# Performance work log

Measured on AMD Instinct MI355X. Metric: run time of the kernel, lower is better.

## Reference

```python
import jax, jax.numpy as jnp
import numpy as np

N_TOKENS = 65536   # number of embeddings to quantize
CODE_DIM = 768     # embedding dim
NUM_CODES = 4096   # codebook size


def setup_inputs() -> dict:
    key = jax.random.key(0)
    k1, k2 = jax.random.split(key)
    x = jax.random.normal(k1, (N_TOKENS, CODE_DIM), dtype=jnp.float32)
    codebook = jax.random.normal(k2, (NUM_CODES, CODE_DIM), dtype=jnp.float32)
    return {"x": x, "codebook": codebook}


def reference(x, codebook):
    # argmin over squared distances == argmin over cdist (sqrt is monotone).
    x2 = jnp.sum(x * x, axis=-1, keepdims=True)          # [N, 1]
    c2 = jnp.sum(codebook * codebook, axis=-1)           # [K]
    dist = x2 + c2[None, :] - 2.0 * jnp.einsum('nd,kd->nk', x, codebook)  # [N, K]
    indices = jnp.argmin(dist, axis=-1)                  # [N] int
    quantized = codebook[indices]                        # gather [N, D]
    # straight-through estimator: forward = quantized, grad flows to x
    q_ste = x + jax.lax.stop_gradient(quantized - x)
    return q_ste, indices
```

## Files before the change

kernel.cpp:

```cpp
#include <hip/hip_runtime.h>

#define N_TOKENS  65536
#define CODE_DIM  768
#define NUM_CODES 4096

#define MARGIN 0.12f
#define FLTMAX 3.4028235e38f

typedef __attribute__((ext_vector_type(8))) _Float16 f16x8;
typedef __attribute__((ext_vector_type(4))) float f32x4;

__device__ __forceinline__ unsigned short f2h(float f) {
  _Float16 h = (_Float16)f;
  return *(unsigned short*)&h;
}
__device__ __forceinline__ void gl2lds16(const void* g, void* l) {
  __builtin_amdgcn_global_load_lds(
      (const __attribute__((address_space(1))) unsigned int*)g,
      (__attribute__((address_space(3))) unsigned int*)l, 16, 0, 0);
}

__global__ __launch_bounds__(256) void vq_convert_kernel(
    const float* __restrict__ x, const float* __restrict__ cb,
    unsigned short* __restrict__ xh, unsigned short* __restrict__ ch,
    float* __restrict__ x2, float* __restrict__ c2, int* __restrict__ fcnt) {
  if (blockIdx.x == 0 && threadIdx.x == 0) *fcnt = 0;
  const int wave = threadIdx.x >> 6;
  const int lane = threadIdx.x & 63;
  const int row  = blockIdx.x * 4 + wave;
  const float* src;
  unsigned short* hdst;
  float* ndst;
  if (row < N_TOKENS) {
    src = x + (size_t)row * CODE_DIM;
    hdst = xh + (size_t)row * CODE_DIM;
    ndst = x2 + row;
  } else {
    const int r = row - N_TOKENS;
    if (r >= NUM_CODES) return;
    src = cb + (size_t)r * CODE_DIM;
    hdst = ch + (size_t)r * CODE_DIM;
    ndst = c2 + r;
  }
  const float4* s4 = (const float4*)src;
  ushort4* h4 = (ushort4*)hdst;
  float acc = 0.f;
#pragma unroll
  for (int i = 0; i < 3; ++i) {
    float4 f = s4[lane + 64 * i];
    ushort4 h;
    h.x = f2h(f.x); h.y = f2h(f.y); h.z = f2h(f.z); h.w = f2h(f.w);
    h4[lane + 64 * i] = h;
    acc += (f.x * f.x + f.y * f.y) + (f.z * f.z + f.w * f.w);
  }
#pragma unroll
  for (int off = 32; off > 0; off >>= 1) acc += __shfl_down(acc, off, 64);
  if (lane == 0) *ndst = acc;
}

#define BT 256
#define KTILE 256
#define NKT (NUM_CODES / KTILE)
#define NST (CODE_DIM / 64)
#define TOT (NKT * NST)

__global__ __launch_bounds__(512, 2) void vq_mfma_kernel(
    const unsigned short* __restrict__ xh, const unsigned short* __restrict__ ch,
    const float* __restrict__ c2, int* __restrict__ out_idx,
    int* __restrict__ fcnt, int* __restrict__ flist) {
  __shared__ __align__(16) unsigned short sA[2][BT * 64];
  __shared__ __align__(16) unsigned short sB[2][KTILE * 64];
  __shared__ float redv[512], redsv[512];
  __shared__ int   redi[512];

  const int tid = threadIdx.x;
  const int wave = tid >> 6, lane = tid & 63;
  const int l15 = lane & 15, quad = lane >> 4;
  const int wr = wave >> 1, wc = wave & 1;
  const int tokBase = blockIdx.x * BT;

  const int lr = lane >> 3;
  const int cSrc = (lane & 7) ^ lr;
  const size_t aOff = (size_t)(tokBase + wave * 32 + lr) * CODE_DIM + cSrc * 8;
  const size_t bOff = (size_t)(wave * 32 + lr) * CODE_DIM + cSrc * 8;

  const int apos = (quad ^ (l15 & 7)) * 8;
  const int aB0 = (wr * 64 + l15) * 64 + apos;
  const int aB1 = (wr * 64 + l15) * 64 + (apos ^ 32);
  const int bB0 = (wc * 128 + l15) * 64 + apos;
  const int bB1 = (wc * 128 + l15) * 64 + (apos ^ 32);

  float v[4][4], sv[4][4];
  int bi[4][4];
#pragma unroll
  for (int i = 0; i < 4; ++i)
#pragma unroll
    for (int r = 0; r < 4; ++r) { v[i][r] = FLTMAX; sv[i][r] = FLTMAX; bi[i][r] = 0; }

  auto STAGE = [&](int slot, int s) {
    const int kw = (s % NST) * 64;
    const size_t rb = (size_t)(s / NST) * (KTILE * (size_t)CODE_DIM);
#pragma unroll
    for (int t = 0; t < 4; ++t)
      gl2lds16(xh + aOff + (size_t)t * (8 * CODE_DIM) + kw,
               &sA[slot][(wave * 32 + t * 8) * 64]);
#pragma unroll
    for (int t = 0; t < 4; ++t)
      gl2lds16(ch + rb + bOff + (size_t)t * (8 * CODE_DIM) + kw,
               &sB[slot][(wave * 32 + t * 8) * 64]);
  };

  STAGE(0, 0);
  asm volatile("s_waitcnt vmcnt(0)" ::: "memory");
  __builtin_amdgcn_s_barrier();
  __builtin_amdgcn_sched_barrier(0);

  for (int kt = 0; kt < NKT; ++kt) {
    f32x4 acc[4][8];
#pragma unroll
    for (int i = 0; i < 4; ++i)
#pragma unroll
      for (int j = 0; j < 8; ++j) acc[i][j] = (f32x4){0.f, 0.f, 0.f, 0.f};

    for (int ks = 0; ks < NST; ++ks) {
      const int gstep = kt * NST + ks;
      const int cur = gstep & 1;
      const unsigned short* As = sA[cur];
      const unsigned short* Bs = sB[cur];
      if (gstep < TOT - 1) STAGE(cur ^ 1, gstep + 1);

      f16x8 fa[4], fb[8];
#pragma unroll
      for (int i = 0; i < 4; ++i) fa[i] = *(const f16x8*)(As + aB0 + i * 1024);
#pragma unroll
      for (int j = 0; j < 8; ++j) fb[j] = *(const f16x8*)(Bs + bB0 + j * 1024);
      __builtin_amdgcn_s_setprio(1);
#pragma unroll
      for (int i = 0; i < 4; ++i)
#pragma unroll
        for (int j = 0; j < 8; ++j)
          acc[i][j] = __builtin_amdgcn_mfma_f32_16x16x32_f16(fa[i], fb[j], acc[i][j], 0, 0, 0);
      __builtin_amdgcn_s_setprio(0);
#pragma unroll
      for (int i = 0; i < 4; ++i) fa[i] = *(const f16x8*)(As + aB1 + i * 1024);
#pragma unroll
      for (int j = 0; j < 8; ++j) fb[j] = *(const f16x8*)(Bs + bB1 + j * 1024);
      __builtin_amdgcn_s_setprio(1);
#pragma unroll
      for (int i = 0; i < 4; ++i)
#pragma unroll
        for (int j = 0; j < 8; ++j)
          acc[i][j] = __builtin_amdgcn_mfma_f32_16x16x32_f16(fa[i], fb[j], acc[i][j], 0, 0, 0);
      __builtin_amdgcn_s_setprio(0);

      asm volatile("s_waitcnt vmcnt(0)" ::: "memory");
      __builtin_amdgcn_s_barrier();
      __builtin_amdgcn_sched_barrier(0);
    }

    const int kbase = kt * KTILE;
#pragma unroll
    for (int j = 0; j < 8; ++j) {
      const int kcol = kbase + wc * 128 + j * 16 + l15;
      const float c2j = c2[kcol];
#pragma unroll
      for (int i = 0; i < 4; ++i)
#pragma unroll
        for (int r = 0; r < 4; ++r) {
          float s = fmaf(-2.0f, acc[i][j][r], c2j);
          float vo = v[i][r];
          sv[i][r] = fminf(sv[i][r], fmaxf(s, vo));
          bool lt = s < vo;
          v[i][r]  = lt ? s : vo;
          bi[i][r] = lt ? kcol : bi[i][r];
        }
    }
  }

#pragma unroll
  for (int i = 0; i < 4; ++i)
#pragma unroll
    for (int r = 0; r < 4; ++r) {
      float vv = v[i][r], svv = sv[i][r];
      int ii = bi[i][r];
#pragma unroll
      for (int m = 1; m < 16; m <<= 1) {
        float ov = __shfl_xor(vv, m, 64);
        float osv = __shfl_xor(svv, m, 64);
        int oi = __shfl_xor(ii, m, 64);
        float nsv = fminf(fminf(svv, osv), fmaxf(vv, ov));
        bool take = (ov < vv) || (ov == vv && oi < ii);
        vv = take ? ov : vv;
        ii = take ? oi : ii;
        svv = nsv;
      }
      if (l15 == 0) {
        int row = wr * 64 + i * 16 + quad * 4 + r;
        redv[row * 2 + wc] = vv;
        redsv[row * 2 + wc] = svv;
        redi[row * 2 + wc] = ii;
      }
    }
  __syncthreads();
  if (tid < 256) {
    float v0 = redv[tid * 2], v1 = redv[tid * 2 + 1];
    float s0 = redsv[tid * 2], s1 = redsv[tid * 2 + 1];
    int i0 = redi[tid * 2], i1 = redi[tid * 2 + 1];
    bool take = (v1 < v0) || (v1 == v0 && i1 < i0);
    float bv = take ? v1 : v0;
    int bidx = take ? i1 : i0;
    float bsv = fminf(fminf(s0, s1), fmaxf(v0, v1));
    out_idx[tokBase + tid] = bidx;
    if (bsv - bv < MARGIN) {
      int p = atomicAdd(fcnt, 1);
      flist[p] = tokBase + tid;
    }
  }
}

__global__ __launch_bounds__(256) void vq_rescan_kernel(
    const float* __restrict__ x, const float* __restrict__ cb,
    const float* __restrict__ x2, const float* __restrict__ c2,
    const int* __restrict__ fcnt, const int* __restrict__ flist,
    int* __restrict__ out_idx) {
  __shared__ float xs[8][CODE_DIM];
  __shared__ float rv[256];
  __shared__ int ri[256];
  const int nf = *fcnt;
  const int ngr = (nf + 7) >> 3;
  for (int g = blockIdx.x; g < ngr; g += gridDim.x) {
    const int base = g * 8;
    int tok[8];
#pragma unroll
    for (int t = 0; t < 8; ++t) tok[t] = flist[min(base + t, nf - 1)];
    __syncthreads();
    if (threadIdx.x < 192) {
#pragma unroll
      for (int t = 0; t < 8; ++t)
        ((float4*)xs[t])[threadIdx.x] =
            ((const float4*)(x + (size_t)tok[t] * CODE_DIM))[threadIdx.x];
    }
    __syncthreads();
    float bv[8]; int bidx[8];
#pragma unroll
    for (int t = 0; t < 8; ++t) { bv[t] = FLTMAX; bidx[t] = 0; }
    for (int kk = 0; kk < NUM_CODES / 256; ++kk) {
      const int k = kk * 256 + threadIdx.x;
      const float4* crow = (const float4*)(cb + (size_t)k * CODE_DIM);
      float a[8];
#pragma unroll
      for (int t = 0; t < 8; ++t) a[t] = 0.f;
      for (int c = 0; c < CODE_DIM / 4; ++c) {
        float4 cv = crow[c];
#pragma unroll
        for (int t = 0; t < 8; ++t) {
          float4 xv = ((float4*)xs[t])[c];
          a[t] += (xv.x * cv.x + xv.y * cv.y) + (xv.z * cv.z + xv.w * cv.w);
        }
      }
      const float c2k = c2[k];
#pragma unroll
      for (int t = 0; t < 8; ++t) {
        float d = (x2[tok[t]] + c2k) - 2.0f * a[t];
        if (d < bv[t]) { bv[t] = d; bidx[t] = k; }
      }
    }
#pragma unroll
    for (int t = 0; t < 8; ++t) {
      __syncthreads();
      rv[threadIdx.x] = bv[t];
      ri[threadIdx.x] = bidx[t];
      __syncthreads();
      for (int s = 128; s > 0; s >>= 1) {
        if (threadIdx.x < s) {
          float ov = rv[threadIdx.x + s];
          int oi = ri[threadIdx.x + s];
          if (ov < rv[threadIdx.x] ||
              (ov == rv[threadIdx.x] && oi < ri[threadIdx.x])) {
            rv[threadIdx.x] = ov;
            ri[threadIdx.x] = oi;
          }
        }
        __syncthreads();
      }
      if (threadIdx.x == 0 && base + t < nf) out_idx[tok[t]] = ri[0];
    }
  }
}

__global__ __launch_bounds__(256) void vq_gather_kernel(
    const float* __restrict__ cb, const int* __restrict__ idx,
    float* __restrict__ out) {
  const int wave = threadIdx.x >> 6;
  const int lane = threadIdx.x & 63;
  const int token = blockIdx.x * 4 + wave;
  const int k = idx[token];
  const float4* src = (const float4*)(cb + (size_t)k * CODE_DIM);
  float4* dst = (float4*)(out + (size_t)token * CODE_DIM);
#pragma unroll
  for (int i = 0; i < 3; ++i) dst[lane + 64 * i] = src[lane + 64 * i];
  if (lane == 0) out[(size_t)N_TOKENS * CODE_DIM + token] = (float)k;
}

#define MT 64
#define KT 128
#define DT 32
#define LDSTRIDE 36

__global__ __launch_bounds__(256) void vq_norms_kernel(
    const float* __restrict__ x, const float* __restrict__ cb,
    float* __restrict__ x2, float* __restrict__ c2) {
  const int wave = threadIdx.x >> 6;
  const int lane = threadIdx.x & 63;
  const int row = blockIdx.x * 4 + wave;
  const float* src;
  float* dst;
  if (row < N_TOKENS) {
    src = x + (size_t)row * CODE_DIM;
    dst = x2 + row;
  } else {
    const int r = row - N_TOKENS;
    if (r >= NUM_CODES) return;
    src = cb + (size_t)r * CODE_DIM;
    dst = c2 + r;
  }
  const float4* s4 = (const float4*)src;
  float acc = 0.f;
#pragma unroll
  for (int i = 0; i < 3; ++i) {
    float4 vv = s4[lane + 64 * i];
    acc += (vv.x * vv.x + vv.y * vv.y) + (vv.z * vv.z + vv.w * vv.w);
  }
#pragma unroll
  for (int off = 32; off > 0; off >>= 1) acc += __shfl_down(acc, off, 64);
  if (lane == 0) *dst = acc;
}

__global__ __launch_bounds__(256) void vq_argmin_kernel(
    const float* __restrict__ x, const float* __restrict__ cb,
    const float* __restrict__ x2, const float* __restrict__ c2,
    int* __restrict__ out_idx) {
  __shared__ float xs[MT * LDSTRIDE];
  __shared__ float cs[KT * LDSTRIDE];
  __shared__ float x2s[MT];
  __shared__ float c2s[KT];
  const int tid = threadIdx.x;
  const int tx = tid & 15;
  const int ty = tid >> 4;
  const int tokBase = blockIdx.x * MT;
  if (tid < MT) x2s[tid] = x2[tokBase + tid];
  float bestv[4];
  int besti[4];
#pragma unroll
  for (int i = 0; i < 4; ++i) { bestv[i] = FLTMAX; besti[i] = 0; }
  const float4* xg = (const float4*)x;
  const float4* cg = (const float4*)cb;
  for (int kt = 0; kt < NUM_CODES / KT; ++kt) {
    const int kBase = kt * KT;
    __syncthreads();
    if (tid < KT) c2s[tid] = c2[kBase + tid];
    float acc[4][8];
#pragma unroll
    for (int i = 0; i < 4; ++i)
#pragma unroll
      for (int j = 0; j < 8; ++j) acc[i][j] = 0.f;
    for (int dc = 0; dc < CODE_DIM / DT; ++dc) {
      __syncthreads();
#pragma unroll
      for (int r = 0; r < 2; ++r) {
        int fidx = tid + 256 * r;
        int row = fidx >> 3, c4 = fidx & 7;
        float4 vv = xg[(size_t)(tokBase + row) * (CODE_DIM / 4) + dc * 8 + c4];
        *(float4*)&xs[row * LDSTRIDE + c4 * 4] = vv;
      }
#pragma unroll
      for (int r = 0; r < 4; ++r) {
        int fidx = tid + 256 * r;
        int row = fidx >> 3, c4 = fidx & 7;
        float4 vv = cg[(size_t)(kBase + row) * (CODE_DIM / 4) + dc * 8 + c4];
        *(float4*)&cs[row * LDSTRIDE + c4 * 4] = vv;
      }
      __syncthreads();
#pragma unroll
      for (int dd = 0; dd < DT / 4; ++dd) {
        float4 xv[4], cv[8];
#pragma unroll
        for (int i = 0; i < 4; ++i)
          xv[i] = *(const float4*)&xs[(ty + 16 * i) * LDSTRIDE + dd * 4];
#pragma unroll
        for (int j = 0; j < 8; ++j)
          cv[j] = *(const float4*)&cs[(tx + 16 * j) * LDSTRIDE + dd * 4];
#pragma unroll
        for (int i = 0; i < 4; ++i)
#pragma unroll
          for (int j = 0; j < 8; ++j)
            acc[i][j] += (xv[i].x * cv[j].x + xv[i].y * cv[j].y) +
                         (xv[i].z * cv[j].z + xv[i].w * cv[j].w);
      }
    }
#pragma unroll
    for (int i = 0; i < 4; ++i) {
      const float xx = x2s[ty + 16 * i];
#pragma unroll
      for (int j = 0; j < 8; ++j) {
        float dist = (xx + c2s[tx + 16 * j]) - 2.0f * acc[i][j];
        int k = kBase + tx + 16 * j;
        if (dist < bestv[i]) { bestv[i] = dist; besti[i] = k; }
      }
    }
  }
  __syncthreads();
  float* rdv = xs;
  int* rdi = (int*)cs;
#pragma unroll
  for (int i = 0; i < 4; ++i) {
    const int m = ty + 16 * i;
    rdv[m * 16 + tx] = bestv[i];
    rdi[m * 16 + tx] = besti[i];
  }
  __syncthreads();
  if (tid < MT) {
    float bv = rdv[tid * 16];
    int bidx = rdi[tid * 16];
#pragma unroll
    for (int t = 1; t < 16; ++t) {
      float vv = rdv[tid * 16 + t];
      int kk = rdi[tid * 16 + t];
      if (vv < bv || (vv == bv && kk < bidx)) { bv = vv; bidx = kk; }
    }
    out_idx[tokBase + tid] = bidx;
  }
}

extern "C" void kernel_launch(void* const* d_in, const int* in_sizes, int n_in,
                              void* d_out, int out_size, void* d_ws, size_t ws_size,
                              hipStream_t stream) {
  (void)in_sizes; (void)n_in; (void)out_size;
  const float* x = (const float*)d_in[0];
  const float* cb = (const float*)d_in[1];
  float* out = (float*)d_out;

  char* w = (char*)d_ws;
  unsigned short* xh = (unsigned short*)w;  w += (size_t)N_TOKENS * CODE_DIM * 2;
  unsigned short* ch = (unsigned short*)w;  w += (size_t)NUM_CODES * CODE_DIM * 2;
  float* x2 = (float*)w;  w += (size_t)N_TOKENS * 4;
  float* c2 = (float*)w;  w += (size_t)NUM_CODES * 4;
  int* idx = (int*)w;     w += (size_t)N_TOKENS * 4;
  int* flist = (int*)w;   w += (size_t)N_TOKENS * 4;
  int* fcnt = (int*)w;    w += 256;
  const size_t need = (size_t)(w - (char*)d_ws);

  if (ws_size >= need) {
    vq_convert_kernel<<<(N_TOKENS + NUM_CODES) / 4, 256, 0, stream>>>(
        x, cb, xh, ch, x2, c2, fcnt);
    vq_mfma_kernel<<<N_TOKENS / BT, 512, 0, stream>>>(
        xh, ch, c2, idx, fcnt, flist);
    vq_rescan_kernel<<<512, 256, 0, stream>>>(x, cb, x2, c2, fcnt, flist, idx);
    vq_gather_kernel<<<N_TOKENS / 4, 256, 0, stream>>>(cb, idx, out);
  } else {
    float* fx2 = (float*)d_ws;
    float* fc2 = fx2 + N_TOKENS;
    int* fidx = (int*)(fc2 + NUM_CODES);
    vq_norms_kernel<<<(N_TOKENS + NUM_CODES + 3) / 4, 256, 0, stream>>>(x, cb, fx2, fc2);
    vq_argmin_kernel<<<N_TOKENS / MT, 256, 0, stream>>>(x, cb, fx2, fc2, fidx);
    vq_gather_kernel<<<N_TOKENS / 4, 256, 0, stream>>>(cb, fidx, out);
  }
}
```

Measured before the change: 1.728 ms.

## Tile codebook through LDS in rescan kernel and split tokens across thread halves

The fp32 rescan kernel used to have each thread stream its own codebook row directly from global memory. It now cooperatively stages 128-code by 96-dim tiles in padded shared memory. Each half of the block handles 4 of the 8 tokens against 128 codes, and the final argmin reduction is split per half. The aim is coalesced codebook loads and less uncoalesced global traffic, at the cost of more barriers per tile and half as many codes per block iteration.

Result: slower. 2.412 ms (+39.6%).

```diff
diff --git a/kernel.cpp b/kernel.cpp
--- a/kernel.cpp
+++ b/kernel.cpp
@@ -218,72 +218,93 @@
   }
 }
 
+#define RT 8
+#define RC 128
+#define RD 96
+#define RSTR 100
+
 __global__ __launch_bounds__(256) void vq_rescan_kernel(
     const float* __restrict__ x, const float* __restrict__ cb,
     const float* __restrict__ x2, const float* __restrict__ c2,
     const int* __restrict__ fcnt, const int* __restrict__ flist,
     int* __restrict__ out_idx) {
-  __shared__ float xs[8][CODE_DIM];
+  __shared__ float xs[RT][CODE_DIM];
+  __shared__ float cs[RC * RSTR];
   __shared__ float rv[256];
-  __shared__ int ri[256];
+  __shared__ int   ri[256];
+  const int tid = threadIdx.x;
+  const int tx = tid & 127;
+  const int ty = tid >> 7;
   const int nf = *fcnt;
-  const int ngr = (nf + 7) >> 3;
+  const int ngr = (nf + RT - 1) / RT;
   for (int g = blockIdx.x; g < ngr; g += gridDim.x) {
-    const int base = g * 8;
-    int tok[8];
-#pragma unroll
-    for (int t = 0; t < 8; ++t) tok[t] = flist[min(base + t, nf - 1)];
+    const int base = g * RT;
+    int tok[RT];
+#pragma unroll
+    for (int t = 0; t < RT; ++t) tok[t] = flist[min(base + t, nf - 1)];
     __syncthreads();
-    if (threadIdx.x < 192) {
-#pragma unroll
-      for (int t = 0; t < 8; ++t)
-        ((float4*)xs[t])[threadIdx.x] =
-            ((const float4*)(x + (size_t)tok[t] * CODE_DIM))[threadIdx.x];
-    }
+    if (tid < 192) {
+#pragma unroll
+      for (int t = 0; t < RT; ++t)
+        ((float4*)xs[t])[tid] =
+            ((const float4*)(x + (size_t)tok[t] * CODE_DIM))[tid];
+    }
+    float xxl[4];
+#pragma unroll
+    for (int r = 0; r < 4; ++r) xxl[r] = x2[tok[ty * 4 + r]];
+    float bv[4]; int bidx[4];
+#pragma unroll
+    for (int r = 0; r < 4; ++r) { bv[r] = FLTMAX; bidx[r] = 0; }
     __syncthreads();
-    float bv[8]; int bidx[8];
-#pragma unroll
-    for (int t = 0; t < 8; ++t) { bv[t] = FLTMAX; bidx[t] = 0; }
-    for (int kk = 0; kk < NUM_CODES / 256; ++kk) {
-      const int k = kk * 256 + threadIdx.x;
-      const float4* crow = (const float4*)(cb + (size_t)k * CODE_DIM);
-      float a[8];
-#pragma unroll
-      for (int t = 0; t < 8; ++t) a[t] = 0.f;
-      for (int c = 0; c < CODE_DIM / 4; ++c) {
-        float4 cv = crow[c];
-#pragma unroll
-        for (int t = 0; t < 8; ++t) {
-          float4 xv = ((float4*)xs[t])[c];
-          a[t] += (xv.x * cv.x + xv.y * cv.y) + (xv.z * cv.z + xv.w * cv.w);
+
+    for (int kt2 = 0; kt2 < NUM_CODES / RC; ++kt2) {
+      const int kBase = kt2 * RC;
+      float acc[4] = {0.f, 0.f, 0.f, 0.f};
+      for (int dc = 0; dc < CODE_DIM / RD; ++dc) {
+        __syncthreads();
+#pragma unroll
+        for (int rr = 0; rr < 12; ++rr) {
+          const int fidx = tid + 256 * rr;
+          const int row = fidx / 24, c4 = fidx % 24;
+          *(float4*)&cs[row * RSTR + c4 * 4] =
+              ((const float4*)(cb + (size_t)(kBase + row) * CODE_DIM + dc * RD))[c4];
         }
-      }
-      const float c2k = c2[k];
-#pragma unroll
-      for (int t = 0; t < 8; ++t) {
-        float d = (x2[tok[t]] + c2k) - 2.0f * a[t];
-        if (d < bv[t]) { bv[t] = d; bidx[t] = k; }
-      }
-    }
-#pragma unroll
-    for (int t = 0; t < 8; ++t) {
+        __syncthreads();
+        const float4* cv4 = (const float4*)&cs[tx * RSTR];
+        const int xb = dc * (RD / 4);
+#pragma unroll
+        for (int dd = 0; dd < RD / 4; ++dd) {
+          const float4 cv = cv4[dd];
+#pragma unroll
+          for (int r = 0; r < 4; ++r) {
+            const float4 xv = ((const float4*)xs[ty * 4 + r])[xb + dd];
+            acc[r] += (xv.x * cv.x + xv.y * cv.y) + (xv.z * cv.z + xv.w * cv.w);
+          }
+        }
+      }
+      const float c2k = c2[kBase + tx];
+#pragma unroll
+      for (int r = 0; r < 4; ++r) {
+        const float d = (xxl[r] + c2k) - 2.0f * acc[r];
+        if (d < bv[r]) { bv[r] = d; bidx[r] = kBase + tx; }
+      }
+    }
+#pragma unroll
+    for (int r = 0; r < 4; ++r) {
       __syncthreads();
-      rv[threadIdx.x] = bv[t];
-      ri[threadIdx.x] = bidx[t];
+      rv[tid] = bv[r]; ri[tid] = bidx[r];
       __syncthreads();
-      for (int s = 128; s > 0; s >>= 1) {
-        if (threadIdx.x < s) {
-          float ov = rv[threadIdx.x + s];
-          int oi = ri[threadIdx.x + s];
-          if (ov < rv[threadIdx.x] ||
-              (ov == rv[threadIdx.x] && oi < ri[threadIdx.x])) {
-            rv[threadIdx.x] = ov;
-            ri[threadIdx.x] = oi;
+      for (int s = 64; s > 0; s >>= 1) {
+        if (tx < s) {
+          const float ov = rv[tid + s];
+          const int oi = ri[tid + s];
+          if (ov < rv[tid] || (ov == rv[tid] && oi < ri[tid])) {
+            rv[tid] = ov; ri[tid] = oi;
           }
         }
         __syncthreads();
       }
-      if (threadIdx.x == 0 && base + t < nf) out_idx[tok[t]] = ri[0];
+      if (tx == 0 && base + ty * 4 + r < nf) out_idx[tok[ty * 4 + r]] = ri[tid];
     }
   }
 }
```
